# Kernel tuning notes

Hardware: AMD Instinct MI355X
Metric: run time of the kernel (lower is better)

## Reference

```python
import jax, jax.numpy as jnp
import numpy as np

N_NODES = 100000
N_EDGES = 250000
EMB = 32
NUM_RELS2 = 100   # 2 * num_rels
NUM_TYPES = 16


def _xavier(key, shape):
    fan_in, fan_out = shape[-2], shape[-1]
    limit = float(np.sqrt(6.0 / (fan_in + fan_out)))
    return jax.random.uniform(key, shape, jnp.float32, -limit, limit)


def setup_inputs() -> dict:
    key = jax.random.key(0)
    ks = jax.random.split(key, 9)
    src_ids = jax.random.randint(ks[0], (N_NODES,), 0, N_NODES)
    edge_src = jax.random.randint(ks[1], (N_EDGES,), 0, N_NODES)
    edge_dst = jax.random.randint(ks[2], (N_EDGES,), 0, N_NODES)
    etype = jax.random.randint(ks[3], (N_EDGES,), 0, NUM_RELS2)
    entity = _xavier(ks[4], (N_NODES, EMB))
    W1 = _xavier(ks[5], (NUM_RELS2, EMB, EMB))
    W2 = _xavier(ks[6], (NUM_RELS2, EMB, NUM_TYPES))
    lambda_w = _xavier(ks[7], (NUM_TYPES, 1))
    lambda_b = jnp.zeros((1,), jnp.float32)
    return {
        "entity": entity, "W1": W1, "W2": W2,
        "lambda_w": lambda_w, "lambda_b": lambda_b,
        "src_ids": src_ids, "edge_src": edge_src,
        "edge_dst": edge_dst, "etype": etype,
    }


def _rgcn_layer(h, W, edge_src, edge_dst, etype, n_dst, activation):
    # gather per-edge relation weights [E, in, out] and per-edge bmm (as DGL does)
    msg = jnp.einsum('ed,edo->eo', h[edge_src], W[etype])  # [E, out]
    s = jax.ops.segment_sum(msg, edge_dst, num_segments=n_dst)  # [N, out]
    deg = jax.ops.segment_sum(jnp.ones((msg.shape[0],), msg.dtype),
                              edge_dst, num_segments=n_dst)
    out = s / jnp.maximum(deg, 1.0)[:, None]  # mean; 0 for isolated dst nodes
    if activation is not None:
        out = activation(out)
    return out


def reference(entity, W1, W2, lambda_w, lambda_b,
              src_ids, edge_src, edge_dst, etype):
    # eval mode: dropout disabled; self_loop=False, bias=False
    h = entity[src_ids]                                            # [N, EMB]
    h = _rgcn_layer(h, W1, edge_src, edge_dst, etype, N_NODES, jax.nn.relu)
    h = _rgcn_layer(h, W2, edge_src, edge_dst, etype, N_NODES, None)  # [N, T]
    # PonderNet loop, max_steps=2: step1 lambda from linear+sigmoid, step2 lambda=1
    lam = jax.nn.sigmoid(h @ lambda_w + lambda_b)[:, 0]            # [N]
    p = jnp.stack([lam, 1.0 - lam])                                # [2, N]
    # recomputed h at step 2 is identical (same params, no dropout)
    y = jnp.stack([h, h])                                          # [2, N, T]
    return (y, p)
```

## Files before the change

kernel.cpp:

```cpp
#include <hip/hip_runtime.h>
#include <hip/hip_bf16.h>

#define N_NODES 100000
#define N_EDGES 250000
#define EMB 32
#define TYPES 16
#define R2 100
#define SB 1024
#define NB ((N_EDGES + SB - 1) / SB)
#define NBN ((N_NODES + SB - 1) / SB)
#define S1 64
#define S2 64

typedef __attribute__((ext_vector_type(8))) short short8;
typedef __attribute__((ext_vector_type(4))) float f32x4;

__device__ __forceinline__ unsigned short f2bf_u(float f) {
    unsigned u = __float_as_uint(f);
    u = (u + 0x7fffu + ((u >> 16) & 1u)) >> 16;
    return (unsigned short)u;
}
__device__ __forceinline__ float bfl(unsigned u) { return __uint_as_float(u << 16); }
__device__ __forceinline__ float bfh(unsigned u) { return __uint_as_float(u & 0xffff0000u); }

__device__ __forceinline__ int wave_incl_scan(int v, int lane) {
#pragma unroll
    for (int o = 1; o < 64; o <<= 1) {
        int x = __shfl_up(v, o);
        if (lane >= o) v += x;
    }
    return v;
}

__global__ __launch_bounds__(SB) void hist_conv_kernel(
        const int* __restrict__ etype, const int* __restrict__ edge_dst,
        const float* __restrict__ entity,
        int* __restrict__ counts, int* __restrict__ dcnt,
        unsigned short* __restrict__ ent_bf) {
    __shared__ int lh[R2];
    int t = threadIdx.x, b = blockIdx.x;
    if (t < R2) lh[t] = 0;
    __syncthreads();
    int e = b * SB + t;
    if (e < N_EDGES) {
        atomicAdd(&lh[etype[e]], 1);
        atomicAdd(&dcnt[edge_dst[e]], 1);
    }
    if (e < 2 * N_NODES) {
        int node = e >> 1, half = e & 1;
        const float4* src = (const float4*)(entity + (size_t)node * EMB + half * 16);
        ushort4* dst = (ushort4*)(ent_bf + (size_t)node * EMB + half * 16);
#pragma unroll
        for (int i = 0; i < 4; ++i) {
            float4 v = src[i];
            ushort4 o = { f2bf_u(v.x), f2bf_u(v.y), f2bf_u(v.z), f2bf_u(v.w) };
            dst[i] = o;
        }
    }
    __syncthreads();
    if (t < R2) counts[b * R2 + t] = lh[t];
}

__global__ __launch_bounds__(SB) void scan_fused_kernel(
        const int* __restrict__ dcnt, int* __restrict__ dstart,
        int* __restrict__ partials,
        const int* __restrict__ counts, int* __restrict__ basem,
        int* __restrict__ total,
        const float* __restrict__ W1, const float* __restrict__ W2,
        unsigned short* __restrict__ pw1, unsigned short* __restrict__ pw2) {
    __shared__ int ws[16];
    int t = threadIdx.x, b = blockIdx.x;
    int lane = t & 63, w = t >> 6;
    if (b < NBN) {
        int i = b * SB + t;
        int v = (i < N_NODES) ? dcnt[i] : 0;
        int inc = wave_incl_scan(v, lane);
        if (lane == 63) ws[w] = inc;
        __syncthreads();
        if (t < 16) {
            int s = ws[t];
            int inc2 = s;
#pragma unroll
            for (int o = 1; o < 16; o <<= 1) {
                int x = __shfl_up(inc2, o);
                if (t >= o) inc2 += x;
            }
            ws[t] = inc2;
        }
        __syncthreads();
        int base = (w == 0) ? 0 : ws[w - 1];
        if (i < N_NODES) dstart[i] = base + inc - v;
        if (t == SB - 1) partials[b] = ws[15];
    } else {
        int r = b - NBN;
        int v = (t < NB) ? counts[t * R2 + r] : 0;
        int inc = wave_incl_scan(v, lane);
        if (lane == 63) ws[w] = inc;
        __syncthreads();
        if (t < 16) {
            int s = ws[t];
            int inc2 = s;
#pragma unroll
            for (int o = 1; o < 16; o <<= 1) {
                int x = __shfl_up(inc2, o);
                if (t >= o) inc2 += x;
            }
            ws[t] = inc2;
        }
        __syncthreads();
        int base = (w == 0) ? 0 : ws[w - 1];
        if (t < NB) basem[t * R2 + r] = base + inc - v;
        if (t == 0) total[r] = ws[15];

        const float* Wr1 = W1 + (size_t)r * (EMB * EMB);
        {
            int l = t >> 4, j = t & 15;
            int n = l & 15, q = l >> 4;
            int k = q * 8 + (j & 7);
            int col = 2 * n + (j >> 3);
            pw1[(size_t)r * 1024 + t] = f2bf_u(Wr1[k * EMB + col]);
        }
        if (t < 512) {
            const float* Wr2 = W2 + (size_t)r * (EMB * TYPES);
            int l = t >> 3, j = t & 7;
            int n = l & 15, q = l >> 4;
            int k = q * 8 + j;
            pw2[(size_t)r * 512 + t] = f2bf_u(Wr2[k * TYPES + n]);
        }
    }
}

__global__ __launch_bounds__(SB) void scatter_kernel(
        const int* __restrict__ edge_src, const int* __restrict__ edge_dst,
        const int* __restrict__ etype, const int* __restrict__ src_ids,
        const int* __restrict__ basem, const int* __restrict__ total,
        const int* __restrict__ partials, const int* __restrict__ dstart,
        int* __restrict__ dcur,
        int* __restrict__ sid, int* __restrict__ srcn, int* __restrict__ pdst,
        int* __restrict__ off_g, int* __restrict__ psg) {
    __shared__ int lh[R2];
    __shared__ int off_s[R2 + 1];
    __shared__ int ps_s[NBN];
    int t = threadIdx.x, b = blockIdx.x;
    int lane = t & 63, w = t >> 6;
    if (t < R2) lh[t] = 0;
    if (w == 0) {
        int a = (lane < R2) ? total[lane] : 0;
        int ai = wave_incl_scan(a, lane);
        int t0 = __shfl(ai, 63);
        int i2 = lane + 64;
        int c = (i2 < R2) ? total[i2] : 0;
        int ci = wave_incl_scan(c, lane) + t0;
        off_s[lane] = ai - a;
        if (i2 < R2) off_s[i2] = ci - c;
        if (i2 == R2 - 1) off_s[R2] = ci;
        if (b == 0) {
            off_g[lane] = ai - a;
            if (i2 < R2) off_g[i2] = ci - c;
            if (i2 == R2 - 1) off_g[R2] = ci;
        }
    } else if (w == 1) {
        int a = (lane < NBN) ? partials[lane] : 0;
        int ai = wave_incl_scan(a, lane);
        int t0 = __shfl(ai, 63);
        int i2 = lane + 64;
        int c = (i2 < NBN) ? partials[i2] : 0;
        int ci = wave_incl_scan(c, lane) + t0;
        ps_s[lane] = ai - a;
        if (i2 < NBN) ps_s[i2] = ci - c;
        if (b == 0) {
            psg[lane] = ai - a;
            if (i2 < NBN) psg[i2] = ci - c;
        }
    }
    __syncthreads();
    int e = b * SB + t;
    if (e >= N_EDGES) return;
    int r = etype[e];
    int rank = atomicAdd(&lh[r], 1);
    int relpos = off_s[r] + basem[b * R2 + r] + rank;
    int d = edge_dst[e];
    int drank = atomicAdd(&dcur[d], 1);
    int s = edge_src[e];
    sid[relpos] = src_ids[s];
    srcn[relpos] = s;
    pdst[relpos] = dstart[d] + ps_s[d >> 10] + drank;
}

__global__ __launch_bounds__(64) void layer1_kernel(
        const unsigned short* __restrict__ ent_bf,
        const unsigned short* __restrict__ pw1,
        const int* __restrict__ off_g, const int* __restrict__ sid,
        const int* __restrict__ pdst, unsigned int* __restrict__ msg1) {
    int r = blockIdx.x % R2, stripe = blockIdx.x / R2;
    int lo = off_g[r], hi = off_g[r + 1];
    int nT = (hi - lo + 15) >> 4;
    int lane = threadIdx.x;
    int n = lane & 15, q = lane >> 4;
    short8 b0 = *(const short8*)(pw1 + (size_t)r * 1024 + lane * 16);
    short8 b1 = *(const short8*)(pw1 + (size_t)r * 1024 + lane * 16 + 8);
    for (int g = stripe; g < nT; g += S1) {
        int base = lo + g * 16;
        int cl = hi - base;
        int me = n < cl ? n : cl - 1;
        int sv = sid[base + me];
        short8 a = *(const short8*)(ent_bf + (size_t)sv * EMB + q * 8);
        f32x4 c0 = {0.f,0.f,0.f,0.f}, c1 = {0.f,0.f,0.f,0.f};
        c0 = __builtin_amdgcn_mfma_f32_16x16x32_bf16(a, b0, c0, 0, 0, 0);
        c1 = __builtin_amdgcn_mfma_f32_16x16x32_bf16(a, b1, c1, 0, 0, 0);
#pragma unroll
        for (int i = 0; i < 4; ++i) {
            int row = q * 4 + i;
            if (row < cl) {
                int p = pdst[base + row];
                msg1[(size_t)p * 16 + n] =
                    (unsigned)f2bf_u(c0[i]) | ((unsigned)f2bf_u(c1[i]) << 16);
            }
        }
    }
}

__global__ void reduce1_kernel(const unsigned int* __restrict__ msg1,
                               const int* __restrict__ dstart,
                               const int* __restrict__ psg,
                               const int* __restrict__ dcnt,
                               unsigned int* __restrict__ h1bf) {
    int t = blockIdx.x * blockDim.x + threadIdx.x;
    if (t >= N_NODES * 16) return;
    int nn = t >> 4, cp = t & 15;
    int s = dstart[nn] + psg[nn >> 10];
    int cnt = dcnt[nn];
    float sx = 0.f, sy = 0.f;
    for (int k = 0; k < cnt; ++k) {
        unsigned v = msg1[(size_t)(s + k) * 16 + cp];
        sx += bfl(v); sy += bfh(v);
    }
    float inv = 1.0f / fmaxf((float)cnt, 1.0f);
    unsigned lo = f2bf_u(fmaxf(sx * inv, 0.f));
    unsigned hi = f2bf_u(fmaxf(sy * inv, 0.f));
    h1bf[t] = lo | (hi << 16);
}

__global__ __launch_bounds__(64) void layer2_kernel(
        const unsigned short* __restrict__ h1bf,
        const unsigned short* __restrict__ pw2,
        const int* __restrict__ off_g, const int* __restrict__ srcn,
        const int* __restrict__ pdst, unsigned short* __restrict__ msg2) {
    int r = blockIdx.x % R2, stripe = blockIdx.x / R2;
    int lo = off_g[r], hi = off_g[r + 1];
    int nT = (hi - lo + 15) >> 4;
    int lane = threadIdx.x;
    int n = lane & 15, q = lane >> 4;
    short8 b = *(const short8*)(pw2 + (size_t)r * 512 + lane * 8);
    for (int g = stripe; g < nT; g += S2) {
        int base = lo + g * 16;
        int cl = hi - base;
        int me = n < cl ? n : cl - 1;
        int s = srcn[base + me];
        short8 a = *(const short8*)(h1bf + (size_t)s * EMB + q * 8);
        f32x4 c = {0.f,0.f,0.f,0.f};
        c = __builtin_amdgcn_mfma_f32_16x16x32_bf16(a, b, c, 0, 0, 0);
#pragma unroll
        for (int i = 0; i < 4; ++i) {
            int row = q * 4 + i;
            if (row < cl) {
                int p = pdst[base + row];
                msg2[(size_t)p * TYPES + n] = f2bf_u(c[i]);
            }
        }
    }
}

__global__ void reduce2_head_kernel(const unsigned int* __restrict__ msg2,
                                    const int* __restrict__ dstart,
                                    const int* __restrict__ psg,
                                    const int* __restrict__ dcnt,
                                    const float* __restrict__ lw,
                                    const float* __restrict__ lb,
                                    float* __restrict__ out) {
    int nn = blockIdx.x * blockDim.x + threadIdx.x;
    if (nn >= N_NODES) return;
    int s = dstart[nn] + psg[nn >> 10];
    int cnt = dcnt[nn];

    float h[TYPES];
#pragma unroll
    for (int j = 0; j < TYPES; ++j) h[j] = 0.f;
    for (int k = 0; k < cnt; ++k) {
        const uint4* row = (const uint4*)(msg2 + (size_t)(s + k) * 8);
        uint4 A = row[0], B = row[1];
        h[0] += bfl(A.x);  h[1] += bfh(A.x);  h[2] += bfl(A.y);  h[3] += bfh(A.y);
        h[4] += bfl(A.z);  h[5] += bfh(A.z);  h[6] += bfl(A.w);  h[7] += bfh(A.w);
        h[8] += bfl(B.x);  h[9] += bfh(B.x);  h[10] += bfl(B.y); h[11] += bfh(B.y);
        h[12] += bfl(B.z); h[13] += bfh(B.z); h[14] += bfl(B.w); h[15] += bfh(B.w);
    }
    float inv = 1.0f / fmaxf((float)cnt, 1.0f);
    float dot = 0.f;
#pragma unroll
    for (int j = 0; j < TYPES; ++j) { h[j] *= inv; dot += h[j] * lw[j]; }
    dot += lb[0];
    float lam = 1.0f / (1.0f + expf(-dot));

    float4* y0 = (float4*)(out + (size_t)nn * TYPES);
    float4* y1 = (float4*)(out + (size_t)N_NODES * TYPES + (size_t)nn * TYPES);
#pragma unroll
    for (int j = 0; j < 4; ++j) {
        float4 v = { h[4*j], h[4*j+1], h[4*j+2], h[4*j+3] };
        y0[j] = v; y1[j] = v;
    }
    out[(size_t)2 * N_NODES * TYPES + nn] = lam;
    out[(size_t)2 * N_NODES * TYPES + N_NODES + nn] = 1.0f - lam;
}

extern "C" void kernel_launch(void* const* d_in, const int* in_sizes, int n_in,
                              void* d_out, int out_size, void* d_ws, size_t ws_size,
                              hipStream_t stream) {
    const float* entity = (const float*)d_in[0];
    const float* W1     = (const float*)d_in[1];
    const float* W2     = (const float*)d_in[2];
    const float* lw     = (const float*)d_in[3];
    const float* lb     = (const float*)d_in[4];
    const int* src_ids  = (const int*)d_in[5];
    const int* edge_src = (const int*)d_in[6];
    const int* edge_dst = (const int*)d_in[7];
    const int* etype    = (const int*)d_in[8];
    float* out = (float*)d_out;

    unsigned int* W = (unsigned int*)d_ws;
    int* dcnt      = (int*)(W + 0);
    int* dcur      = (int*)(W + 100000);
    int* dstart    = (int*)(W + 200000);
    int* partials  = (int*)(W + 300008);
    int* counts    = (int*)(W + 300136);
    int* basem     = (int*)(W + 324636);
    int* total     = (int*)(W + 349136);
    int* off_g     = (int*)(W + 349264);
    int* psg       = (int*)(W + 349392);
    int* sid       = (int*)(W + 349520);
    int* srcn      = (int*)(W + 599520);
    int* pdst      = (int*)(W + 849520);
    unsigned short* ent_bf = (unsigned short*)(W + 1099520);
    unsigned short* pw1    = (unsigned short*)(W + 2699520);
    unsigned short* pw2    = (unsigned short*)(W + 2750720);
    unsigned int* msg1     = (unsigned int*)(W + 2776320);
    unsigned int* h1bf     = (unsigned int*)(W + 6776320);
    unsigned int* msg2     = (unsigned int*)(W + 8376320);

    (void)hipMemsetAsync(d_ws, 0, 200000 * sizeof(int), stream);

    hist_conv_kernel<<<NB, SB, 0, stream>>>(etype, edge_dst, entity,
                                            counts, dcnt, ent_bf);
    scan_fused_kernel<<<NBN + R2, SB, 0, stream>>>(dcnt, dstart, partials,
                                                   counts, basem, total,
                                                   W1, W2, pw1, pw2);
    scatter_kernel<<<NB, SB, 0, stream>>>(edge_src, edge_dst, etype, src_ids,
                                          basem, total, partials, dstart, dcur,
                                          sid, srcn, pdst, off_g, psg);
    layer1_kernel<<<R2 * S1, 64, 0, stream>>>(ent_bf, pw1, off_g, sid, pdst, msg1);
    reduce1_kernel<<<(N_NODES * 16 + 255) / 256, 256, 0, stream>>>(
        msg1, dstart, psg, dcnt, h1bf);
    layer2_kernel<<<R2 * S2, 64, 0, stream>>>((const unsigned short*)h1bf, pw2,
                                              off_g, srcn, pdst,
                                              (unsigned short*)msg2);
    reduce2_head_kernel<<<(N_NODES + 255) / 256, 256, 0, stream>>>(
        msg2, dstart, psg, dcnt, lw, lb, out);
}
```

Baseline: 153.9 us.

## Fuse all pipeline stages into one cooperative persistent kernel with grid syncs

Replaces the memset and seven separate kernel launches with a single cooperative kernel of 240 blocks of 1024 threads. Stages are separated by grid-wide barriers, and each stage loops over virtual blocks or wave jobs. The aim is to remove launch gaps and per-kernel ramp-up and tail time between the small dependent stages. In exchange, every stage runs on a fixed grid of 1024-thread blocks, which may limit occupancy, and it pays for about eight grid barriers. The per-relation stripe count is also lowered to 40.

```diff
diff --git a/kernel.cpp b/kernel.cpp
--- a/kernel.cpp
+++ b/kernel.cpp
@@ -1,5 +1,7 @@
 #include <hip/hip_runtime.h>
-#include <hip/hip_bf16.h>
+#include <hip/hip_cooperative_groups.h>
+
+namespace cg = cooperative_groups;
 
 #define N_NODES 100000
 #define N_EDGES 250000
@@ -7,10 +9,12 @@
 #define TYPES 16
 #define R2 100
 #define SB 1024
-#define NB ((N_EDGES + SB - 1) / SB)
-#define NBN ((N_NODES + SB - 1) / SB)
-#define S1 64
-#define S2 64
+#define NB 245
+#define NBN 98
+#define GRID 240
+#define BLK 1024
+#define SPR1 40
+#define SPR2 40
 
 typedef __attribute__((ext_vector_type(8))) short short8;
 typedef __attribute__((ext_vector_type(4))) float f32x4;
@@ -32,336 +36,305 @@
     return v;
 }
 
-__global__ __launch_bounds__(SB) void hist_conv_kernel(
-        const int* __restrict__ etype, const int* __restrict__ edge_dst,
-        const float* __restrict__ entity,
-        int* __restrict__ counts, int* __restrict__ dcnt,
-        unsigned short* __restrict__ ent_bf) {
+struct P {
+    const float *entity, *W1, *W2, *lw, *lb;
+    const int *src_ids, *edge_src, *edge_dst, *etype;
+    float* out;
+    int *dcnt, *dcur, *dstart, *partials, *counts, *basem, *total, *off_g, *psg;
+    int *sid, *srcn, *pdst;
+    unsigned short *ent_bf, *pw1, *pw2;
+    unsigned int *msg1, *h1bf, *msg2;
+};
+
+__global__ __launch_bounds__(BLK) void mega_kernel(P p) {
+    cg::grid_group gg = cg::this_grid();
     __shared__ int lh[R2];
-    int t = threadIdx.x, b = blockIdx.x;
-    if (t < R2) lh[t] = 0;
-    __syncthreads();
-    int e = b * SB + t;
-    if (e < N_EDGES) {
-        atomicAdd(&lh[etype[e]], 1);
-        atomicAdd(&dcnt[edge_dst[e]], 1);
-    }
-    if (e < 2 * N_NODES) {
-        int node = e >> 1, half = e & 1;
-        const float4* src = (const float4*)(entity + (size_t)node * EMB + half * 16);
-        ushort4* dst = (ushort4*)(ent_bf + (size_t)node * EMB + half * 16);
-#pragma unroll
-        for (int i = 0; i < 4; ++i) {
-            float4 v = src[i];
+    __shared__ int ws[16];
+    const int t = threadIdx.x, b = blockIdx.x;
+    const int lane = t & 63, w = t >> 6;
+    const int gtid = b * BLK + t;
+    const int NT = GRID * BLK;
+    const int waveId = b * (BLK / 64) + w;
+    const int NW = GRID * (BLK / 64);
+
+    for (int i = gtid; i < 2 * N_NODES; i += NT) p.dcnt[i] = 0;
+    gg.sync();
+
+    for (int i = gtid; i < 2 * N_NODES; i += NT) {
+        int node = i >> 1, half = i & 1;
+        const float4* src = (const float4*)(p.entity + (size_t)node * EMB + half * 16);
+        ushort4* dst = (ushort4*)(p.ent_bf + (size_t)node * EMB + half * 16);
+#pragma unroll
+        for (int k2 = 0; k2 < 4; ++k2) {
+            float4 v = src[k2];
             ushort4 o = { f2bf_u(v.x), f2bf_u(v.y), f2bf_u(v.z), f2bf_u(v.w) };
-            dst[i] = o;
-        }
-    }
-    __syncthreads();
-    if (t < R2) counts[b * R2 + t] = lh[t];
-}
-
-__global__ __launch_bounds__(SB) void scan_fused_kernel(
-        const int* __restrict__ dcnt, int* __restrict__ dstart,
-        int* __restrict__ partials,
-        const int* __restrict__ counts, int* __restrict__ basem,
-        int* __restrict__ total,
-        const float* __restrict__ W1, const float* __restrict__ W2,
-        unsigned short* __restrict__ pw1, unsigned short* __restrict__ pw2) {
-    __shared__ int ws[16];
-    int t = threadIdx.x, b = blockIdx.x;
-    int lane = t & 63, w = t >> 6;
-    if (b < NBN) {
-        int i = b * SB + t;
-        int v = (i < N_NODES) ? dcnt[i] : 0;
-        int inc = wave_incl_scan(v, lane);
-        if (lane == 63) ws[w] = inc;
-        __syncthreads();
-        if (t < 16) {
-            int s = ws[t];
-            int inc2 = s;
-#pragma unroll
-            for (int o = 1; o < 16; o <<= 1) {
-                int x = __shfl_up(inc2, o);
-                if (t >= o) inc2 += x;
-            }
-            ws[t] = inc2;
-        }
-        __syncthreads();
-        int base = (w == 0) ? 0 : ws[w - 1];
-        if (i < N_NODES) dstart[i] = base + inc - v;
-        if (t == SB - 1) partials[b] = ws[15];
-    } else {
-        int r = b - NBN;
-        int v = (t < NB) ? counts[t * R2 + r] : 0;
-        int inc = wave_incl_scan(v, lane);
-        if (lane == 63) ws[w] = inc;
-        __syncthreads();
-        if (t < 16) {
-            int s = ws[t];
-            int inc2 = s;
-#pragma unroll
-            for (int o = 1; o < 16; o <<= 1) {
-                int x = __shfl_up(inc2, o);
-                if (t >= o) inc2 += x;
-            }
-            ws[t] = inc2;
-        }
-        __syncthreads();
-        int base = (w == 0) ? 0 : ws[w - 1];
-        if (t < NB) basem[t * R2 + r] = base + inc - v;
-        if (t == 0) total[r] = ws[15];
-
-        const float* Wr1 = W1 + (size_t)r * (EMB * EMB);
-        {
-            int l = t >> 4, j = t & 15;
-            int n = l & 15, q = l >> 4;
-            int k = q * 8 + (j & 7);
-            int col = 2 * n + (j >> 3);
-            pw1[(size_t)r * 1024 + t] = f2bf_u(Wr1[k * EMB + col]);
-        }
-        if (t < 512) {
-            const float* Wr2 = W2 + (size_t)r * (EMB * TYPES);
-            int l = t >> 3, j = t & 7;
-            int n = l & 15, q = l >> 4;
-            int k = q * 8 + j;
-            pw2[(size_t)r * 512 + t] = f2bf_u(Wr2[k * TYPES + n]);
-        }
-    }
-}
-
-__global__ __launch_bounds__(SB) void scatter_kernel(
-        const int* __restrict__ edge_src, const int* __restrict__ edge_dst,
-        const int* __restrict__ etype, const int* __restrict__ src_ids,
-        const int* __restrict__ basem, const int* __restrict__ total,
-        const int* __restrict__ partials, const int* __restrict__ dstart,
-        int* __restrict__ dcur,
-        int* __restrict__ sid, int* __restrict__ srcn, int* __restrict__ pdst,
-        int* __restrict__ off_g, int* __restrict__ psg) {
-    __shared__ int lh[R2];
-    __shared__ int off_s[R2 + 1];
-    __shared__ int ps_s[NBN];
-    int t = threadIdx.x, b = blockIdx.x;
-    int lane = t & 63, w = t >> 6;
-    if (t < R2) lh[t] = 0;
-    if (w == 0) {
-        int a = (lane < R2) ? total[lane] : 0;
-        int ai = wave_incl_scan(a, lane);
-        int t0 = __shfl(ai, 63);
-        int i2 = lane + 64;
-        int c = (i2 < R2) ? total[i2] : 0;
-        int ci = wave_incl_scan(c, lane) + t0;
-        off_s[lane] = ai - a;
-        if (i2 < R2) off_s[i2] = ci - c;
-        if (i2 == R2 - 1) off_s[R2] = ci;
-        if (b == 0) {
-            off_g[lane] = ai - a;
-            if (i2 < R2) off_g[i2] = ci - c;
-            if (i2 == R2 - 1) off_g[R2] = ci;
-        }
-    } else if (w == 1) {
-        int a = (lane < NBN) ? partials[lane] : 0;
-        int ai = wave_incl_scan(a, lane);
-        int t0 = __shfl(ai, 63);
-        int i2 = lane + 64;
-        int c = (i2 < NBN) ? partials[i2] : 0;
-        int ci = wave_incl_scan(c, lane) + t0;
-        ps_s[lane] = ai - a;
-        if (i2 < NBN) ps_s[i2] = ci - c;
-        if (b == 0) {
-            psg[lane] = ai - a;
-            if (i2 < NBN) psg[i2] = ci - c;
-        }
-    }
-    __syncthreads();
-    int e = b * SB + t;
-    if (e >= N_EDGES) return;
-    int r = etype[e];
-    int rank = atomicAdd(&lh[r], 1);
-    int relpos = off_s[r] + basem[b * R2 + r] + rank;
-    int d = edge_dst[e];
-    int drank = atomicAdd(&dcur[d], 1);
-    int s = edge_src[e];
-    sid[relpos] = src_ids[s];
-    srcn[relpos] = s;
-    pdst[relpos] = dstart[d] + ps_s[d >> 10] + drank;
-}
-
-__global__ __launch_bounds__(64) void layer1_kernel(
-        const unsigned short* __restrict__ ent_bf,
-        const unsigned short* __restrict__ pw1,
-        const int* __restrict__ off_g, const int* __restrict__ sid,
-        const int* __restrict__ pdst, unsigned int* __restrict__ msg1) {
-    int r = blockIdx.x % R2, stripe = blockIdx.x / R2;
-    int lo = off_g[r], hi = off_g[r + 1];
-    int nT = (hi - lo + 15) >> 4;
-    int lane = threadIdx.x;
-    int n = lane & 15, q = lane >> 4;
-    short8 b0 = *(const short8*)(pw1 + (size_t)r * 1024 + lane * 16);
-    short8 b1 = *(const short8*)(pw1 + (size_t)r * 1024 + lane * 16 + 8);
-    for (int g = stripe; g < nT; g += S1) {
-        int base = lo + g * 16;
-        int cl = hi - base;
-        int me = n < cl ? n : cl - 1;
-        int sv = sid[base + me];
-        short8 a = *(const short8*)(ent_bf + (size_t)sv * EMB + q * 8);
-        f32x4 c0 = {0.f,0.f,0.f,0.f}, c1 = {0.f,0.f,0.f,0.f};
-        c0 = __builtin_amdgcn_mfma_f32_16x16x32_bf16(a, b0, c0, 0, 0, 0);
-        c1 = __builtin_amdgcn_mfma_f32_16x16x32_bf16(a, b1, c1, 0, 0, 0);
-#pragma unroll
-        for (int i = 0; i < 4; ++i) {
-            int row = q * 4 + i;
-            if (row < cl) {
-                int p = pdst[base + row];
-                msg1[(size_t)p * 16 + n] =
-                    (unsigned)f2bf_u(c0[i]) | ((unsigned)f2bf_u(c1[i]) << 16);
-            }
-        }
-    }
-}
-
-__global__ void reduce1_kernel(const unsigned int* __restrict__ msg1,
-                               const int* __restrict__ dstart,
-                               const int* __restrict__ psg,
-                               const int* __restrict__ dcnt,
-                               unsigned int* __restrict__ h1bf) {
-    int t = blockIdx.x * blockDim.x + threadIdx.x;
-    if (t >= N_NODES * 16) return;
-    int nn = t >> 4, cp = t & 15;
-    int s = dstart[nn] + psg[nn >> 10];
-    int cnt = dcnt[nn];
-    float sx = 0.f, sy = 0.f;
-    for (int k = 0; k < cnt; ++k) {
-        unsigned v = msg1[(size_t)(s + k) * 16 + cp];
-        sx += bfl(v); sy += bfh(v);
-    }
-    float inv = 1.0f / fmaxf((float)cnt, 1.0f);
-    unsigned lo = f2bf_u(fmaxf(sx * inv, 0.f));
-    unsigned hi = f2bf_u(fmaxf(sy * inv, 0.f));
-    h1bf[t] = lo | (hi << 16);
-}
-
-__global__ __launch_bounds__(64) void layer2_kernel(
-        const unsigned short* __restrict__ h1bf,
-        const unsigned short* __restrict__ pw2,
-        const int* __restrict__ off_g, const int* __restrict__ srcn,
-        const int* __restrict__ pdst, unsigned short* __restrict__ msg2) {
-    int r = blockIdx.x % R2, stripe = blockIdx.x / R2;
-    int lo = off_g[r], hi = off_g[r + 1];
-    int nT = (hi - lo + 15) >> 4;
-    int lane = threadIdx.x;
-    int n = lane & 15, q = lane >> 4;
-    short8 b = *(const short8*)(pw2 + (size_t)r * 512 + lane * 8);
-    for (int g = stripe; g < nT; g += S2) {
-        int base = lo + g * 16;
-        int cl = hi - base;
-        int me = n < cl ? n : cl - 1;
-        int s = srcn[base + me];
-        short8 a = *(const short8*)(h1bf + (size_t)s * EMB + q * 8);
-        f32x4 c = {0.f,0.f,0.f,0.f};
-        c = __builtin_amdgcn_mfma_f32_16x16x32_bf16(a, b, c, 0, 0, 0);
-#pragma unroll
-        for (int i = 0; i < 4; ++i) {
-            int row = q * 4 + i;
-            if (row < cl) {
-                int p = pdst[base + row];
-                msg2[(size_t)p * TYPES + n] = f2bf_u(c[i]);
-            }
-        }
-    }
-}
-
-__global__ void reduce2_head_kernel(const unsigned int* __restrict__ msg2,
-                                    const int* __restrict__ dstart,
-                                    const int* __restrict__ psg,
-                                    const int* __restrict__ dcnt,
-                                    const float* __restrict__ lw,
-                                    const float* __restrict__ lb,
-                                    float* __restrict__ out) {
-    int nn = blockIdx.x * blockDim.x + threadIdx.x;
-    if (nn >= N_NODES) return;
-    int s = dstart[nn] + psg[nn >> 10];
-    int cnt = dcnt[nn];
-
-    float h[TYPES];
-#pragma unroll
-    for (int j = 0; j < TYPES; ++j) h[j] = 0.f;
-    for (int k = 0; k < cnt; ++k) {
-        const uint4* row = (const uint4*)(msg2 + (size_t)(s + k) * 8);
-        uint4 A = row[0], B = row[1];
-        h[0] += bfl(A.x);  h[1] += bfh(A.x);  h[2] += bfl(A.y);  h[3] += bfh(A.y);
-        h[4] += bfl(A.z);  h[5] += bfh(A.z);  h[6] += bfl(A.w);  h[7] += bfh(A.w);
-        h[8] += bfl(B.x);  h[9] += bfh(B.x);  h[10] += bfl(B.y); h[11] += bfh(B.y);
-        h[12] += bfl(B.z); h[13] += bfh(B.z); h[14] += bfl(B.w); h[15] += bfh(B.w);
-    }
-    float inv = 1.0f / fmaxf((float)cnt, 1.0f);
-    float dot = 0.f;
-#pragma unroll
-    for (int j = 0; j < TYPES; ++j) { h[j] *= inv; dot += h[j] * lw[j]; }
-    dot += lb[0];
-    float lam = 1.0f / (1.0f + expf(-dot));
-
-    float4* y0 = (float4*)(out + (size_t)nn * TYPES);
-    float4* y1 = (float4*)(out + (size_t)N_NODES * TYPES + (size_t)nn * TYPES);
-#pragma unroll
-    for (int j = 0; j < 4; ++j) {
-        float4 v = { h[4*j], h[4*j+1], h[4*j+2], h[4*j+3] };
-        y0[j] = v; y1[j] = v;
-    }
-    out[(size_t)2 * N_NODES * TYPES + nn] = lam;
-    out[(size_t)2 * N_NODES * TYPES + N_NODES + nn] = 1.0f - lam;
+            dst[k2] = o;
+        }
+    }
+    for (int vb = b; vb < NB; vb += GRID) {
+        __syncthreads();
+        if (t < R2) lh[t] = 0;
+        __syncthreads();
+        int e = vb * SB + t;
+        if (e < N_EDGES) {
+            atomicAdd(&lh[p.etype[e]], 1);
+            atomicAdd(&p.dcnt[p.edge_dst[e]], 1);
+        }
+        __syncthreads();
+        if (t < R2) p.counts[vb * R2 + t] = lh[t];
+    }
+    gg.sync();
+
+    for (int vb = b; vb < NBN + R2; vb += GRID) {
+        if (vb < NBN) {
+            int i = vb * SB + t;
+            int v = (i < N_NODES) ? p.dcnt[i] : 0;
+            int inc = wave_incl_scan(v, lane);
+            __syncthreads();
+            if (lane == 63) ws[w] = inc;
+            __syncthreads();
+            if (t < 16) {
+                int s2 = ws[t];
+#pragma unroll
+                for (int o = 1; o < 16; o <<= 1) {
+                    int x = __shfl_up(s2, o);
+                    if (t >= o) s2 += x;
+                }
+                ws[t] = s2;
+            }
+            __syncthreads();
+            int base = (w == 0) ? 0 : ws[w - 1];
+            if (i < N_NODES) p.dstart[i] = base + inc - v;
+            if (t == 0) p.partials[vb] = ws[15];
+        } else {
+            int r = vb - NBN;
+            int v = (t < NB) ? p.counts[t * R2 + r] : 0;
+            int inc = wave_incl_scan(v, lane);
+            __syncthreads();
+            if (lane == 63) ws[w] = inc;
+            __syncthreads();
+            if (t < 16) {
+                int s2 = ws[t];
+#pragma unroll
+                for (int o = 1; o < 16; o <<= 1) {
+                    int x = __shfl_up(s2, o);
+                    if (t >= o) s2 += x;
+                }
+                ws[t] = s2;
+            }
+            __syncthreads();
+            int base = (w == 0) ? 0 : ws[w - 1];
+            if (t < NB) p.basem[t * R2 + r] = base + inc - v;
+            if (t == 0) p.total[r] = ws[15];
+
+            const float* Wr1 = p.W1 + (size_t)r * (EMB * EMB);
+            {
+                int l = t >> 4, j = t & 15;
+                int n = l & 15, q = l >> 4;
+                int k = q * 8 + (j & 7);
+                int col = 2 * n + (j >> 3);
+                p.pw1[(size_t)r * 1024 + t] = f2bf_u(Wr1[k * EMB + col]);
+            }
+            if (t < 512) {
+                const float* Wr2 = p.W2 + (size_t)r * (EMB * TYPES);
+                int l = t >> 3, j = t & 7;
+                int n = l & 15, q = l >> 4;
+                int k = q * 8 + j;
+                p.pw2[(size_t)r * 512 + t] = f2bf_u(Wr2[k * TYPES + n]);
+            }
+        }
+    }
+    gg.sync();
+
+    if (b == 0) {
+        if (w == 0) {
+            int a = (lane < R2) ? p.total[lane] : 0;
+            int ai = wave_incl_scan(a, lane);
+            int t0 = __shfl(ai, 63);
+            int i2 = lane + 64;
+            int c = (i2 < R2) ? p.total[i2] : 0;
+            int ci = wave_incl_scan(c, lane) + t0;
+            p.off_g[lane] = ai - a;
+            if (i2 < R2) p.off_g[i2] = ci - c;
+            if (i2 == R2 - 1) p.off_g[R2] = ci;
+        } else if (w == 1) {
+            int a = (lane < NBN) ? p.partials[lane] : 0;
+            int ai = wave_incl_scan(a, lane);
+            int t0 = __shfl(ai, 63);
+            int i2 = lane + 64;
+            int c = (i2 < NBN) ? p.partials[i2] : 0;
+            int ci = wave_incl_scan(c, lane) + t0;
+            p.psg[lane] = ai - a;
+            if (i2 < NBN) p.psg[i2] = ci - c;
+        }
+    }
+    gg.sync();
+
+    for (int vb = b; vb < NB; vb += GRID) {
+        __syncthreads();
+        if (t < R2) lh[t] = 0;
+        __syncthreads();
+        int e = vb * SB + t;
+        if (e < N_EDGES) {
+            int r = p.etype[e];
+            int rank = atomicAdd(&lh[r], 1);
+            int relpos = p.off_g[r] + p.basem[vb * R2 + r] + rank;
+            int d = p.edge_dst[e];
+            int drank = atomicAdd(&p.dcur[d], 1);
+            int s = p.edge_src[e];
+            p.sid[relpos] = p.src_ids[s];
+            p.srcn[relpos] = s;
+            p.pdst[relpos] = p.dstart[d] + p.psg[d >> 10] + drank;
+        }
+    }
+    gg.sync();
+
+    {
+        int n = lane & 15, q = lane >> 4;
+        for (int job = waveId; job < R2 * SPR1; job += NW) {
+            int r = job % R2, stripe = job / R2;
+            int lo = p.off_g[r], hi = p.off_g[r + 1];
+            int nT = (hi - lo + 15) >> 4;
+            short8 b0 = *(const short8*)(p.pw1 + (size_t)r * 1024 + lane * 16);
+            short8 b1 = *(const short8*)(p.pw1 + (size_t)r * 1024 + lane * 16 + 8);
+            for (int g = stripe; g < nT; g += SPR1) {
+                int base = lo + g * 16;
+                int cl = hi - base;
+                int me = n < cl ? n : cl - 1;
+                int sv = p.sid[base + me];
+                short8 a = *(const short8*)(p.ent_bf + (size_t)sv * EMB + q * 8);
+                f32x4 c0 = {0.f,0.f,0.f,0.f}, c1 = {0.f,0.f,0.f,0.f};
+                c0 = __builtin_amdgcn_mfma_f32_16x16x32_bf16(a, b0, c0, 0, 0, 0);
+                c1 = __builtin_amdgcn_mfma_f32_16x16x32_bf16(a, b1, c1, 0, 0, 0);
+#pragma unroll
+                for (int i = 0; i < 4; ++i) {
+                    int row = q * 4 + i;
+                    if (row < cl) {
+                        int pp = p.pdst[base + row];
+                        p.msg1[(size_t)pp * 16 + n] =
+                            (unsigned)f2bf_u(c0[i]) | ((unsigned)f2bf_u(c1[i]) << 16);
+                    }
+                }
+            }
+        }
+    }
+    gg.sync();
+
+    for (int i = gtid; i < N_NODES * 16; i += NT) {
+        int nn = i >> 4, cp = i & 15;
+        int s = p.dstart[nn] + p.psg[nn >> 10];
+        int cnt = p.dcnt[nn];
+        float sx = 0.f, sy = 0.f;
+        for (int k = 0; k < cnt; ++k) {
+            unsigned v = p.msg1[(size_t)(s + k) * 16 + cp];
+            sx += bfl(v); sy += bfh(v);
+        }
+        float inv = 1.0f / fmaxf((float)cnt, 1.0f);
+        unsigned lo2 = f2bf_u(fmaxf(sx * inv, 0.f));
+        unsigned hi2 = f2bf_u(fmaxf(sy * inv, 0.f));
+        p.h1bf[i] = lo2 | (hi2 << 16);
+    }
+    gg.sync();
+
+    {
+        int n = lane & 15, q = lane >> 4;
+        const unsigned short* h1u = (const unsigned short*)p.h1bf;
+        unsigned short* m2 = (unsigned short*)p.msg2;
+        for (int job = waveId; job < R2 * SPR2; job += NW) {
+            int r = job % R2, stripe = job / R2;
+            int lo = p.off_g[r], hi = p.off_g[r + 1];
+            int nT = (hi - lo + 15) >> 4;
+            short8 bb = *(const short8*)(p.pw2 + (size_t)r * 512 + lane * 8);
+            for (int g = stripe; g < nT; g += SPR2) {
+                int base = lo + g * 16;
+                int cl = hi - base;
+                int me = n < cl ? n : cl - 1;
+                int s = p.srcn[base + me];
+                short8 a = *(const short8*)(h1u + (size_t)s * EMB + q * 8);
+                f32x4 c = {0.f,0.f,0.f,0.f};
+                c = __builtin_amdgcn_mfma_f32_16x16x32_bf16(a, bb, c, 0, 0, 0);
+#pragma unroll
+                for (int i = 0; i < 4; ++i) {
+                    int row = q * 4 + i;
+                    if (row < cl) {
+                        int pp = p.pdst[base + row];
+                        m2[(size_t)pp * TYPES + n] = f2bf_u(c[i]);
+                    }
+                }
+            }
+        }
+    }
+    gg.sync();
+
+    for (int nn = gtid; nn < N_NODES; nn += NT) {
+        int s = p.dstart[nn] + p.psg[nn >> 10];
+        int cnt = p.dcnt[nn];
+        float h[TYPES];
+#pragma unroll
+        for (int j = 0; j < TYPES; ++j) h[j] = 0.f;
+        for (int k = 0; k < cnt; ++k) {
+            const uint4* row = (const uint4*)(p.msg2 + (size_t)(s + k) * 8);
+            uint4 A = row[0], B = row[1];
+            h[0] += bfl(A.x);  h[1] += bfh(A.x);  h[2] += bfl(A.y);  h[3] += bfh(A.y);
+            h[4] += bfl(A.z);  h[5] += bfh(A.z);  h[6] += bfl(A.w);  h[7] += bfh(A.w);
+            h[8] += bfl(B.x);  h[9] += bfh(B.x);  h[10] += bfl(B.y); h[11] += bfh(B.y);
+            h[12] += bfl(B.z); h[13] += bfh(B.z); h[14] += bfl(B.w); h[15] += bfh(B.w);
+        }
+        float inv = 1.0f / fmaxf((float)cnt, 1.0f);
+        float dot = 0.f;
+#pragma unroll
+        for (int j = 0; j < TYPES; ++j) { h[j] *= inv; dot += h[j] * p.lw[j]; }
+        dot += p.lb[0];
+        float lam = 1.0f / (1.0f + expf(-dot));
+
+        float4* y0 = (float4*)(p.out + (size_t)nn * TYPES);
+        float4* y1 = (float4*)(p.out + (size_t)N_NODES * TYPES + (size_t)nn * TYPES);
+#pragma unroll
+        for (int j = 0; j < 4; ++j) {
+            float4 v = { h[4*j], h[4*j+1], h[4*j+2], h[4*j+3] };
+            y0[j] = v; y1[j] = v;
+        }
+        p.out[(size_t)2 * N_NODES * TYPES + nn] = lam;
+        p.out[(size_t)2 * N_NODES * TYPES + N_NODES + nn] = 1.0f - lam;
+    }
 }
 
 extern "C" void kernel_launch(void* const* d_in, const int* in_sizes, int n_in,
                               void* d_out, int out_size, void* d_ws, size_t ws_size,
                               hipStream_t stream) {
-    const float* entity = (const float*)d_in[0];
-    const float* W1     = (const float*)d_in[1];
-    const float* W2     = (const float*)d_in[2];
-    const float* lw     = (const float*)d_in[3];
-    const float* lb     = (const float*)d_in[4];
-    const int* src_ids  = (const int*)d_in[5];
-    const int* edge_src = (const int*)d_in[6];
-    const int* edge_dst = (const int*)d_in[7];
-    const int* etype    = (const int*)d_in[8];
-    float* out = (float*)d_out;
+    P h;
+    h.entity   = (const float*)d_in[0];
+    h.W1       = (const float*)d_in[1];
+    h.W2       = (const float*)d_in[2];
+    h.lw       = (const float*)d_in[3];
+    h.lb       = (const float*)d_in[4];
+    h.src_ids  = (const int*)d_in[5];
+    h.edge_src = (const int*)d_in[6];
+    h.edge_dst = (const int*)d_in[7];
+    h.etype    = (const int*)d_in[8];
+    h.out      = (float*)d_out;
 
     unsigned int* W = (unsigned int*)d_ws;
-    int* dcnt      = (int*)(W + 0);
-    int* dcur      = (int*)(W + 100000);
-    int* dstart    = (int*)(W + 200000);
-    int* partials  = (int*)(W + 300008);
-    int* counts    = (int*)(W + 300136);
-    int* basem     = (int*)(W + 324636);
-    int* total     = (int*)(W + 349136);
-    int* off_g     = (int*)(W + 349264);
-    int* psg       = (int*)(W + 349392);
-    int* sid       = (int*)(W + 349520);
-    int* srcn      = (int*)(W + 599520);
-    int* pdst      = (int*)(W + 849520);
-    unsigned short* ent_bf = (unsigned short*)(W + 1099520);
-    unsigned short* pw1    = (unsigned short*)(W + 2699520);
-    unsigned short* pw2    = (unsigned short*)(W + 2750720);
-    unsigned int* msg1     = (unsigned int*)(W + 2776320);
-    unsigned int* h1bf     = (unsigned int*)(W + 6776320);
-    unsigned int* msg2     = (unsigned int*)(W + 8376320);
-
-    (void)hipMemsetAsync(d_ws, 0, 200000 * sizeof(int), stream);
-
-    hist_conv_kernel<<<NB, SB, 0, stream>>>(etype, edge_dst, entity,
-                                            counts, dcnt, ent_bf);
-    scan_fused_kernel<<<NBN + R2, SB, 0, stream>>>(dcnt, dstart, partials,
-                                                   counts, basem, total,
-                                                   W1, W2, pw1, pw2);
-    scatter_kernel<<<NB, SB, 0, stream>>>(edge_src, edge_dst, etype, src_ids,
-                                          basem, total, partials, dstart, dcur,
-                                          sid, srcn, pdst, off_g, psg);
-    layer1_kernel<<<R2 * S1, 64, 0, stream>>>(ent_bf, pw1, off_g, sid, pdst, msg1);
-    reduce1_kernel<<<(N_NODES * 16 + 255) / 256, 256, 0, stream>>>(
-        msg1, dstart, psg, dcnt, h1bf);
-    layer2_kernel<<<R2 * S2, 64, 0, stream>>>((const unsigned short*)h1bf, pw2,
-                                              off_g, srcn, pdst,
-                                              (unsigned short*)msg2);
-    reduce2_head_kernel<<<(N_NODES + 255) / 256, 256, 0, stream>>>(
-        msg2, dstart, psg, dcnt, lw, lb, out);
+    h.dcnt     = (int*)(W + 0);
+    h.dcur     = (int*)(W + 100000);
+    h.dstart   = (int*)(W + 200000);
+    h.partials = (int*)(W + 300008);
+    h.counts   = (int*)(W + 300136);
+    h.basem    = (int*)(W + 324636);
+    h.total    = (int*)(W + 349136);
+    h.off_g    = (int*)(W + 349264);
+    h.psg      = (int*)(W + 349392);
+    h.sid      = (int*)(W + 349520);
+    h.srcn     = (int*)(W + 599520);
+    h.pdst     = (int*)(W + 849520);
+    h.ent_bf   = (unsigned short*)(W + 1099520);
+    h.pw1      = (unsigned short*)(W + 2699520);
+    h.pw2      = (unsigned short*)(W + 2750720);
+    h.msg1     = (unsigned int*)(W + 2776320);
+    h.h1bf     = (unsigned int*)(W + 6776320);
+    h.msg2     = (unsigned int*)(W + 8376320);
+
+    void* args[] = { (void*)&h };
+    (void)hipLaunchCooperativeKernel((const void*)mega_kernel, dim3(GRID), dim3(BLK),
+                                     args, 0, stream);
 }
```

Result: slower. 414.5 us (+169.2%).
